# Performance work log

Hardware: AMD Instinct MI355X
Metric: run time of the kernel (lower is better)

Reference implementation:

```python
import jax, jax.numpy as jnp
import numpy as np

EMBED_DIM = 1024
NUM_HEADS = 16
HEAD_DIM = EMBED_DIM // NUM_HEADS


def setup_inputs() -> dict:
    key = jax.random.key(0)
    kx, kq, kk, kv, ko = jax.random.split(key, 5)
    scale = 1.0 / np.sqrt(EMBED_DIM)
    return {
        "x": jax.random.normal(kx, (4, 2048, EMBED_DIM), dtype=jnp.float32),
        # nn.Linear weights are [out, in]; y = x @ W.T
        "w_q": jax.random.normal(kq, (EMBED_DIM, EMBED_DIM), dtype=jnp.float32) * scale,
        "w_k": jax.random.normal(kk, (EMBED_DIM, EMBED_DIM), dtype=jnp.float32) * scale,
        "w_v": jax.random.normal(kv, (EMBED_DIM, EMBED_DIM), dtype=jnp.float32) * scale,
        "w_o": jax.random.normal(ko, (EMBED_DIM, EMBED_DIM), dtype=jnp.float32) * scale,
    }


def reference(x, w_q, w_k, w_v, w_o):
    b, s, _ = x.shape
    # projections (Linear with no bias: x @ W.T)
    q = (x @ w_q.T).reshape(b, s, NUM_HEADS, HEAD_DIM).transpose(0, 2, 1, 3)
    k = (x @ w_k.T).reshape(b, s, NUM_HEADS, HEAD_DIM).transpose(0, 2, 1, 3)
    v = (x @ w_v.T).reshape(b, s, NUM_HEADS, HEAD_DIM).transpose(0, 2, 1, 3)
    # scores: [b, h, s, s]
    scores = jnp.einsum("bhqd,bhkd->bhqk", q, k) / jnp.sqrt(jnp.float32(HEAD_DIM)).astype(x.dtype)
    attn = jax.nn.softmax(scores, axis=-1)
    out = jnp.einsum("bhqk,bhkd->bhqd", attn, v)  # [b, h, s, d]
    out = out.transpose(0, 2, 1, 3).reshape(b, s, EMBED_DIM)
    return out @ w_o.T
```

## Files before the change

kernel.cpp:

```cpp
#include <hip/hip_runtime.h>
#include <math.h>

#define EMBED 1024
#define NHEAD 16
#define HDIM  64
#define BATCH 4
#define SEQ   2048
#define MROWS (BATCH * SEQ)

typedef __attribute__((ext_vector_type(8))) short short8;
typedef __attribute__((ext_vector_type(4))) float floatx4;
typedef __attribute__((ext_vector_type(16))) float floatx16;

#if __has_builtin(__builtin_amdgcn_exp2f)
#define EXP2(x) __builtin_amdgcn_exp2f(x)
#else
#define EXP2(x) exp2f(x)
#endif

__device__ __forceinline__ unsigned short f2bf(float f) {
  unsigned u = __float_as_uint(f);
  u += 0x7fffu + ((u >> 16) & 1u);
  return (unsigned short)(u >> 16);
}

__device__ __forceinline__ unsigned pack2bf(float lo, float hi) {
  return ((__float_as_uint(lo) + 0x8000u) >> 16) |
         ((__float_as_uint(hi) + 0x8000u) & 0xffff0000u);
}

__device__ __forceinline__ void gl_lds16(const void* g, void* l) {
  __builtin_amdgcn_global_load_lds(
      (const __attribute__((address_space(1))) unsigned int*)g,
      (__attribute__((address_space(3))) unsigned int*)l, 16, 0, 0);
}

__global__ __launch_bounds__(256) void cast_bf16_kernel(
    const float* __restrict__ x,  const float* __restrict__ wq,
    const float* __restrict__ wk, const float* __restrict__ wv,
    const float* __restrict__ wo,
    unsigned short* __restrict__ xb, unsigned short* __restrict__ wb) {
  const size_t NX = (size_t)MROWS * EMBED;
  size_t i4 = ((size_t)blockIdx.x * 256 + threadIdx.x) * 4;
  const float* src;
  unsigned short* dst;
  size_t off;
  if (i4 < NX) {
    src = x; dst = xb; off = i4;
  } else {
    size_t j = i4 - NX;
    int r = (int)(j >> 20);
    off = j & ((1u << 20) - 1);
    src = (r == 0) ? wq : (r == 1) ? wk : (r == 2) ? wv : wo;
    dst = wb + ((size_t)r << 20);
  }
  float4 v = *(const float4*)(src + off);
  ushort4 o;
  o.x = f2bf(v.x); o.y = f2bf(v.y); o.z = f2bf(v.z); o.w = f2bf(v.w);
  *(ushort4*)(dst + off) = o;
}

__device__ __forceinline__ void gemm_core(
    const unsigned short* __restrict__ Amat,
    const unsigned short* __restrict__ Bmat,
    int mBase, int nBase,
    unsigned short* As, unsigned short* Bs,
    floatx4 acc[4][4]) {
  const int t = threadIdx.x;
  const int lane = t & 63, w = t >> 6;
  const int wr = w >> 1, wc = w & 1;
  const int quad = lane >> 4, l15 = lane & 15;

  const int f0 = (w * 2 + 0) * 64 + lane;
  const int f1 = (w * 2 + 1) * 64 + lane;
  const unsigned short* ga0 = Amat + (size_t)(mBase + (f0 >> 2)) * EMBED + (f0 & 3) * 8;
  const unsigned short* ga1 = Amat + (size_t)(mBase + (f1 >> 2)) * EMBED + (f1 & 3) * 8;
  const unsigned short* gb0 = Bmat + (size_t)(nBase + (f0 >> 2)) * EMBED + (f0 & 3) * 8;
  const unsigned short* gb1 = Bmat + (size_t)(nBase + (f1 >> 2)) * EMBED + (f1 & 3) * 8;
  unsigned short* la0 = As + (w * 2 + 0) * 512;
  unsigned short* la1 = As + (w * 2 + 1) * 512;
  unsigned short* lb0 = Bs + (w * 2 + 0) * 512;
  unsigned short* lb1 = Bs + (w * 2 + 1) * 512;

  for (int kb = 0; kb < EMBED; kb += 32) {
    __syncthreads();
    gl_lds16(ga0 + kb, la0);
    gl_lds16(ga1 + kb, la1);
    gl_lds16(gb0 + kb, lb0);
    gl_lds16(gb1 + kb, lb1);
    __syncthreads();
    short8 a[4], b[4];
#pragma unroll
    for (int mi = 0; mi < 4; ++mi)
      a[mi] = *(const short8*)&As[(wr * 64 + mi * 16 + l15) * 32 + quad * 8];
#pragma unroll
    for (int ni = 0; ni < 4; ++ni)
      b[ni] = *(const short8*)&Bs[(wc * 64 + ni * 16 + l15) * 32 + quad * 8];
#pragma unroll
    for (int mi = 0; mi < 4; ++mi)
#pragma unroll
      for (int ni = 0; ni < 4; ++ni)
        acc[mi][ni] = __builtin_amdgcn_mfma_f32_16x16x32_bf16(
            a[mi], b[ni], acc[mi][ni], 0, 0, 0);
  }
}

__global__ __launch_bounds__(256) void proj_qkv_bf16(
    const unsigned short* __restrict__ xb,
    const unsigned short* __restrict__ wb,
    unsigned short* __restrict__ qkv) {
  const int which = blockIdx.z;
  const unsigned short* W = wb + ((size_t)which << 20);
  const int nBase = blockIdx.x * 128;
  const int mBase = blockIdx.y * 128;

  __shared__ unsigned short As[128 * 32];
  __shared__ unsigned short Bs[128 * 32];

  floatx4 acc[4][4] = {};
  gemm_core(xb, W, mBase, nBase, As, Bs, acc);

  const int t = threadIdx.x;
  const int lane = t & 63, w = t >> 6;
  const int wr = w >> 1, wc = w & 1;
  const int quad = lane >> 4, l15 = lane & 15;

  unsigned short* out = qkv + (size_t)which * MROWS * EMBED;
  if (which < 2) {
    const float scale = (which == 0) ? 0.18033688f : 1.0f;
#pragma unroll
    for (int mi = 0; mi < 4; ++mi)
#pragma unroll
      for (int ni = 0; ni < 4; ++ni) {
        const int n = nBase + wc * 64 + ni * 16 + l15;
        const int h = n >> 6, d = n & 63;
#pragma unroll
        for (int r = 0; r < 4; ++r) {
          const int m = mBase + wr * 64 + mi * 16 + quad * 4 + r;
          const int b = m >> 11, s = m & (SEQ - 1);
          out[(((size_t)(b * NHEAD + h) * SEQ) + s) * HDIM + d] =
              f2bf(acc[mi][ni][r] * scale);
        }
      }
  } else {
#pragma unroll
    for (int mi = 0; mi < 4; ++mi) {
      const int m0 = mBase + wr * 64 + mi * 16 + quad * 4;
      const int b = m0 >> 11, s0 = m0 & (SEQ - 1);
#pragma unroll
      for (int ni = 0; ni < 4; ++ni) {
        const int n = nBase + wc * 64 + ni * 16 + l15;
        const int h = n >> 6, d = n & 63;
        ushort4 pk;
        pk.x = f2bf(acc[mi][ni][0]); pk.y = f2bf(acc[mi][ni][1]);
        pk.z = f2bf(acc[mi][ni][2]); pk.w = f2bf(acc[mi][ni][3]);
        *(ushort4*)&out[((size_t)(b * NHEAD + h) * HDIM + d) * SEQ + s0] = pk;
      }
    }
  }
}

__global__ __launch_bounds__(256) void attn_mfma(
    const unsigned short* __restrict__ qkv,
    unsigned short* __restrict__ aout) {
  const unsigned short* Q = qkv;
  const unsigned short* K = qkv + (size_t)MROWS * EMBED;
  const unsigned short* V = qkv + 2 * (size_t)MROWS * EMBED;

  const int bh = blockIdx.y;
  const int qBase = blockIdx.x * 128;

  __shared__ unsigned short Ks[64 * 64];
  __shared__ unsigned short Vs[64 * 64];

  const int t = threadIdx.x;
  const int lane = t & 63, w = t >> 6;
  const int h2 = lane >> 5;
  const int q31 = lane & 31;

  const unsigned short* qrow =
      Q + ((size_t)bh * SEQ + qBase + w * 32 + q31) * HDIM;
  short8 qa[4];
#pragma unroll
  for (int ds = 0; ds < 4; ++ds)
    qa[ds] = *(const short8*)(qrow + ds * 16 + h2 * 8);

  const int f0 = (w * 2 + 0) * 64 + lane;
  const int f1 = (w * 2 + 1) * 64 + lane;
  const int kr0 = f0 >> 3, kg0 = (f0 & 7) ^ (kr0 & 7);
  const int kr1 = f1 >> 3, kg1 = (f1 & 7) ^ (kr1 & 7);
  const unsigned short* kbase = K + (size_t)bh * SEQ * HDIM;
  const unsigned short* vbase = V + (size_t)bh * HDIM * SEQ;
  const unsigned short* gk0 = kbase + (size_t)kr0 * HDIM + kg0 * 8;
  const unsigned short* gk1 = kbase + (size_t)kr1 * HDIM + kg1 * 8;
  const unsigned short* gv0 = vbase + (size_t)kr0 * SEQ + kg0 * 8;
  const unsigned short* gv1 = vbase + (size_t)kr1 * SEQ + kg1 * 8;
  unsigned short* lk0 = Ks + (w * 2 + 0) * 512;
  unsigned short* lk1 = Ks + (w * 2 + 1) * 512;
  unsigned short* lv0 = Vs + (w * 2 + 0) * 512;
  unsigned short* lv1 = Vs + (w * 2 + 1) * 512;

  floatx16 ot0 = {}, ot1 = {};
  floatx16 osum = {};

  const short one_bf = (short)0x3F80;
  const short8 onesA = {one_bf, one_bf, one_bf, one_bf,
                        one_bf, one_bf, one_bf, one_bf};

  for (int kt = 0; kt < SEQ; kt += 64) {
    __syncthreads();
    gl_lds16(gk0 + (size_t)kt * HDIM, lk0);
    gl_lds16(gk1 + (size_t)kt * HDIM, lk1);
    gl_lds16(gv0 + kt, lv0);
    gl_lds16(gv1 + kt, lv1);
    __syncthreads();

    floatx16 st0 = {}, st1 = {};
#pragma unroll
    for (int ds = 0; ds < 4; ++ds) {
      const int g = ds * 2 + h2;
      short8 ka0 = *(const short8*)&Ks[q31 * 64 + ((g ^ (q31 & 7)) * 8)];
      st0 = __builtin_amdgcn_mfma_f32_32x32x16_bf16(ka0, qa[ds], st0, 0, 0, 0);
      const int k1 = 32 + q31;
      short8 ka1 = *(const short8*)&Ks[k1 * 64 + ((g ^ (k1 & 7)) * 8)];
      st1 = __builtin_amdgcn_mfma_f32_32x32x16_bf16(ka1, qa[ds], st1, 0, 0, 0);
    }

    unsigned pk0[8], pk1[8], sw0[8], sw1[8];
#pragma unroll
    for (int i = 0; i < 8; ++i) {
      pk0[i] = pack2bf(EXP2(st0[2 * i]), EXP2(st0[2 * i + 1]));
      sw0[i] = __shfl_xor(pk0[i], 32);
      pk1[i] = pack2bf(EXP2(st1[2 * i]), EXP2(st1[2 * i + 1]));
      sw1[i] = __shfl_xor(pk1[i], 32);
    }

#pragma unroll
    for (int kst = 0; kst < 4; ++kst) {
      const unsigned* pk = (kst < 2) ? pk0 : pk1;
      const unsigned* sw = (kst < 2) ? sw0 : sw1;
      const int kl = kst & 1;
      union { unsigned u[4]; short8 s; } pb;
      pb.u[0] = h2 ? sw[4 * kl + 2] : pk[4 * kl + 0];
      pb.u[1] = h2 ? sw[4 * kl + 3] : pk[4 * kl + 1];
      pb.u[2] = h2 ? pk[4 * kl + 2] : sw[4 * kl + 0];
      pb.u[3] = h2 ? pk[4 * kl + 3] : sw[4 * kl + 1];

      osum = __builtin_amdgcn_mfma_f32_32x32x16_bf16(onesA, pb.s, osum, 0, 0, 0);

      const int g = kst * 2 + h2;
      short8 va0 = *(const short8*)&Vs[q31 * 64 + ((g ^ (q31 & 7)) * 8)];
      ot0 = __builtin_amdgcn_mfma_f32_32x32x16_bf16(va0, pb.s, ot0, 0, 0, 0);
      const int d1 = 32 + q31;
      short8 va1 = *(const short8*)&Vs[d1 * 64 + ((g ^ (d1 & 7)) * 8)];
      ot1 = __builtin_amdgcn_mfma_f32_32x32x16_bf16(va1, pb.s, ot1, 0, 0, 0);
    }
  }

  const float inv = 1.0f / osum[0];

  const int b = bh >> 4, hh = bh & 15;
  unsigned short* orow =
      aout + ((size_t)b * SEQ + qBase + w * 32 + q31) * EMBED + hh * HDIM;
#pragma unroll
  for (int rg = 0; rg < 4; ++rg) {
    const int d0 = rg * 8 + h2 * 4;
    ushort4 p0, p1;
    p0.x = f2bf(ot0[4 * rg + 0] * inv); p0.y = f2bf(ot0[4 * rg + 1] * inv);
    p0.z = f2bf(ot0[4 * rg + 2] * inv); p0.w = f2bf(ot0[4 * rg + 3] * inv);
    *(ushort4*)(orow + d0) = p0;
    p1.x = f2bf(ot1[4 * rg + 0] * inv); p1.y = f2bf(ot1[4 * rg + 1] * inv);
    p1.z = f2bf(ot1[4 * rg + 2] * inv); p1.w = f2bf(ot1[4 * rg + 3] * inv);
    *(ushort4*)(orow + 32 + d0) = p1;
  }
}

__global__ __launch_bounds__(256) void out_proj_bf16(
    const unsigned short* __restrict__ aout,
    const unsigned short* __restrict__ wb,
    float* __restrict__ Cout) {
  const int nBase = blockIdx.x * 128;
  const int mBase = blockIdx.y * 128;

  __shared__ unsigned short As[128 * 32];
  __shared__ unsigned short Bs[128 * 32];

  floatx4 acc[4][4] = {};
  gemm_core(aout, wb + ((size_t)3 << 20), mBase, nBase, As, Bs, acc);

  const int t = threadIdx.x;
  const int lane = t & 63, w = t >> 6;
  const int wr = w >> 1, wc = w & 1;
  const int quad = lane >> 4, l15 = lane & 15;

#pragma unroll
  for (int mi = 0; mi < 4; ++mi)
#pragma unroll
    for (int ni = 0; ni < 4; ++ni) {
      const int n = nBase + wc * 64 + ni * 16 + l15;
#pragma unroll
      for (int r = 0; r < 4; ++r) {
        const int m = mBase + wr * 64 + mi * 16 + quad * 4 + r;
        Cout[(size_t)m * EMBED + n] = acc[mi][ni][r];
      }
    }
}

extern "C" void kernel_launch(void* const* d_in, const int* in_sizes, int n_in,
                              void* d_out, int out_size, void* d_ws, size_t ws_size,
                              hipStream_t stream) {
  const float* x  = (const float*)d_in[0];
  const float* wq = (const float*)d_in[1];
  const float* wk = (const float*)d_in[2];
  const float* wv = (const float*)d_in[3];
  const float* wo = (const float*)d_in[4];
  float* out = (float*)d_out;

  char* ws = (char*)d_ws;
  unsigned short* xb   = (unsigned short*)(ws);
  unsigned short* wb   = (unsigned short*)(ws + (16u << 20));
  unsigned short* qkv  = (unsigned short*)(ws + (26u << 20));
  unsigned short* aout = (unsigned short*)(ws + (76u << 20));

  cast_bf16_kernel<<<12288, 256, 0, stream>>>(x, wq, wk, wv, wo, xb, wb);
  proj_qkv_bf16<<<dim3(EMBED / 128, MROWS / 128, 3), 256, 0, stream>>>(xb, wb, qkv);
  attn_mfma<<<dim3(SEQ / 128, BATCH * NHEAD), 256, 0, stream>>>(qkv, aout);
  out_proj_bf16<<<dim3(EMBED / 128, MROWS / 128), 256, 0, stream>>>(aout, wb, out);
}
```

Before: 306.2 us.

## Double-buffer K/V tiles in attention, remap blocks per XCD, use packed bf16 convert

The attention kernel now uses two LDS buffers for each K/V tile. It prefetches the next tile with global_load_lds while computing on the current one, which removes one barrier per iteration and overlaps loads with MFMA work. The grid is flattened to 1D and remapped so that all query blocks of a given (batch, head) land on the same XCD, meant to improve L2 reuse of K/V. P packing switches to the hardware cvt_pk_bf16_f32 builtin when it is available. The cost is doubled LDS use and a rounding behaviour that may differ slightly from the old add-and-truncate packing.

```diff
diff --git a/kernel.cpp b/kernel.cpp
--- a/kernel.cpp
+++ b/kernel.cpp
@@ -24,10 +24,19 @@
   return (unsigned short)(u >> 16);
 }
 
+#if __has_builtin(__builtin_amdgcn_cvt_pk_bf16_f32)
+__device__ __forceinline__ unsigned pack2bf(float lo, float hi) {
+  typedef __attribute__((ext_vector_type(2))) __bf16 bf2;
+  union { bf2 b; unsigned u; } c;
+  c.b = __builtin_amdgcn_cvt_pk_bf16_f32(lo, hi);
+  return c.u;
+}
+#else
 __device__ __forceinline__ unsigned pack2bf(float lo, float hi) {
   return ((__float_as_uint(lo) + 0x8000u) >> 16) |
          ((__float_as_uint(hi) + 0x8000u) & 0xffff0000u);
 }
+#endif
 
 __device__ __forceinline__ void gl_lds16(const void* g, void* l) {
   __builtin_amdgcn_global_load_lds(
@@ -167,11 +176,13 @@
   const unsigned short* K = qkv + (size_t)MROWS * EMBED;
   const unsigned short* V = qkv + 2 * (size_t)MROWS * EMBED;
 
-  const int bh = blockIdx.y;
-  const int qBase = blockIdx.x * 128;
-
-  __shared__ unsigned short Ks[64 * 64];
-  __shared__ unsigned short Vs[64 * 64];
+  const int id = blockIdx.x;
+  const int xcd = id & 7, slot = id >> 3;
+  const int bh = xcd * 8 + (slot >> 4);
+  const int qBase = (slot & 15) * 128;
+
+  __shared__ unsigned short Ks[2 * 64 * 64];
+  __shared__ unsigned short Vs[2 * 64 * 64];
 
   const int t = threadIdx.x;
   const int lane = t & 63, w = t >> 6;
@@ -207,22 +218,31 @@
   const short8 onesA = {one_bf, one_bf, one_bf, one_bf,
                         one_bf, one_bf, one_bf, one_bf};
 
+  gl_lds16(gk0, lk0);
+  gl_lds16(gk1, lk1);
+  gl_lds16(gv0, lv0);
+  gl_lds16(gv1, lv1);
+
   for (int kt = 0; kt < SEQ; kt += 64) {
+    const int buf = (kt >> 6) & 1;
+    const int boff = buf * 4096;
     __syncthreads();
-    gl_lds16(gk0 + (size_t)kt * HDIM, lk0);
-    gl_lds16(gk1 + (size_t)kt * HDIM, lk1);
-    gl_lds16(gv0 + kt, lv0);
-    gl_lds16(gv1 + kt, lv1);
-    __syncthreads();
+    if (kt + 64 < SEQ) {
+      const int noff = (boff ^ 4096);
+      gl_lds16(gk0 + (size_t)(kt + 64) * HDIM, lk0 + noff);
+      gl_lds16(gk1 + (size_t)(kt + 64) * HDIM, lk1 + noff);
+      gl_lds16(gv0 + (kt + 64), lv0 + noff);
+      gl_lds16(gv1 + (kt + 64), lv1 + noff);
+    }
 
     floatx16 st0 = {}, st1 = {};
 #pragma unroll
     for (int ds = 0; ds < 4; ++ds) {
       const int g = ds * 2 + h2;
-      short8 ka0 = *(const short8*)&Ks[q31 * 64 + ((g ^ (q31 & 7)) * 8)];
+      short8 ka0 = *(const short8*)&Ks[boff + q31 * 64 + ((g ^ (q31 & 7)) * 8)];
       st0 = __builtin_amdgcn_mfma_f32_32x32x16_bf16(ka0, qa[ds], st0, 0, 0, 0);
       const int k1 = 32 + q31;
-      short8 ka1 = *(const short8*)&Ks[k1 * 64 + ((g ^ (k1 & 7)) * 8)];
+      short8 ka1 = *(const short8*)&Ks[boff + k1 * 64 + ((g ^ (k1 & 7)) * 8)];
       st1 = __builtin_amdgcn_mfma_f32_32x32x16_bf16(ka1, qa[ds], st1, 0, 0, 0);
     }
 
@@ -249,10 +269,10 @@
       osum = __builtin_amdgcn_mfma_f32_32x32x16_bf16(onesA, pb.s, osum, 0, 0, 0);
 
       const int g = kst * 2 + h2;
-      short8 va0 = *(const short8*)&Vs[q31 * 64 + ((g ^ (q31 & 7)) * 8)];
+      short8 va0 = *(const short8*)&Vs[boff + q31 * 64 + ((g ^ (q31 & 7)) * 8)];
       ot0 = __builtin_amdgcn_mfma_f32_32x32x16_bf16(va0, pb.s, ot0, 0, 0, 0);
       const int d1 = 32 + q31;
-      short8 va1 = *(const short8*)&Vs[d1 * 64 + ((g ^ (d1 & 7)) * 8)];
+      short8 va1 = *(const short8*)&Vs[boff + d1 * 64 + ((g ^ (d1 & 7)) * 8)];
       ot1 = __builtin_amdgcn_mfma_f32_32x32x16_bf16(va1, pb.s, ot1, 0, 0, 0);
     }
   }
@@ -324,6 +344,6 @@
 
   cast_bf16_kernel<<<12288, 256, 0, stream>>>(x, wq, wk, wv, wo, xb, wb);
   proj_qkv_bf16<<<dim3(EMBED / 128, MROWS / 128, 3), 256, 0, stream>>>(xb, wb, qkv);
-  attn_mfma<<<dim3(SEQ / 128, BATCH * NHEAD), 256, 0, stream>>>(qkv, aout);
+  attn_mfma<<<1024, 256, 0, stream>>>(qkv, aout);
   out_proj_bf16<<<dim3(EMBED / 128, MROWS / 128), 256, 0, stream>>>(aout, wb, out);
 }
```

After: 320.9 us. +4.8%, slower.
